# Kernel tuning notes

Measured on AMD Instinct MI355X. Metric: run time of the kernel, lower is better.

## Reference

```python
import jax, jax.numpy as jnp
import numpy as np

EMBED = 512
NHEAD = 16
HDIM = EMBED // NHEAD
HIDDEN = 512  # Mlp hidden is hard-coded to 512
EPS_LN = 1e-6
EPS_ATT = 1e-6


def layernorm(x, gamma, beta):
    mu = jnp.mean(x, axis=-1, keepdims=True)
    var = jnp.mean(jnp.square(x - mu), axis=-1, keepdims=True)
    return (x - mu) * jax.lax.rsqrt(var + EPS_LN) * gamma + beta


def setup_inputs() -> dict:
    key = jax.random.key(0)
    ks = jax.random.split(key, 16)
    B, N, C = 8, 4096, EMBED
    s = 1.0 / np.sqrt(C)
    inp = {
        "x": jax.random.normal(ks[0], (B, N, C), dtype=jnp.float32),
        # projection weights stored as (in, out); torch Linear uses x @ W.T
        "Wq": jax.random.normal(ks[1], (C, C), dtype=jnp.float32) * s,
        "Wk": jax.random.normal(ks[2], (C, C), dtype=jnp.float32) * s,
        "Wv": jax.random.normal(ks[3], (C, C), dtype=jnp.float32) * s,
        "Wm": jax.random.normal(ks[4], (C, C), dtype=jnp.float32) * s,
        "W1": jax.random.normal(ks[5], (C, HIDDEN), dtype=jnp.float32) * s,
        "b1": jax.random.normal(ks[6], (HIDDEN,), dtype=jnp.float32) * 1e-6,
        "W2": jax.random.normal(ks[7], (HIDDEN, C), dtype=jnp.float32) * (1.0 / np.sqrt(HIDDEN)),
        "b2": jax.random.normal(ks[8], (C,), dtype=jnp.float32) * 1e-6,
        "g_att": jnp.ones((C,), dtype=jnp.float32),
        "b_att": jnp.zeros((C,), dtype=jnp.float32),
        "g_ffn": jnp.ones((C,), dtype=jnp.float32),
        "b_ffn": jnp.zeros((C,), dtype=jnp.float32),
    }
    return inp


def reference(x, Wq, Wk, Wv, Wm, W1, b1, W2, b2, g_att, b_att, g_ffn, b_ffn):
    B, N, C = x.shape
    # --- attention sub-block ---
    h = layernorm(x, g_att, b_att)
    q = (h @ Wq).reshape(B, N, NHEAD, HDIM)
    k = (h @ Wk).reshape(B, N, NHEAD, HDIM)
    v = (h @ Wv).reshape(B, N, NHEAD, HDIM)
    Q = jax.nn.elu(q) + 1.0  # feature map: elu(x)+1
    K = jax.nn.elu(k) + 1.0
    v = v / N
    KV = jnp.einsum('nshd,nshv->nhdv', K, v)
    Z = 1.0 / (jnp.einsum('nlhd,nhd->nlh', Q, K.sum(axis=1)) + EPS_ATT)
    msg = jnp.einsum('nlhd,nhdv->nlhv', Q, KV) * Z[..., None] * N
    msg = msg.reshape(B, N, C) @ Wm
    x = x + msg
    # --- feed-forward sub-block ---
    h2 = layernorm(x, g_ffn, b_ffn)
    f = jax.nn.gelu(h2 @ W1 + b1, approximate=False) @ W2 + b2
    return x + f
```

## Files before the change

### kernel.cpp

```cpp
#include <hip/hip_runtime.h>
#include <hip/hip_bf16.h>
#include <math.h>

typedef unsigned short u16;
typedef __attribute__((ext_vector_type(8))) __bf16 bf16x8;
typedef __attribute__((ext_vector_type(4))) float floatx4;

#define SEQ   4096
#define BATCH 8
#define ROWS  32768
#define C     512
#define NH    16
#define HD    32

__device__ inline u16 f2bf(float f) {
    union { float f; unsigned u; } v; v.f = f;
    unsigned r = (v.u + 0x7FFFu + ((v.u >> 16) & 1u)) >> 16;
    return (u16)r;
}
__device__ inline float bf2f(u16 h) {
    union { unsigned u; float f; } v; v.u = ((unsigned)h) << 16;
    return v.f;
}

__device__ inline void g2lds16(const u16* g, u16* l) {
    __builtin_amdgcn_global_load_lds((const __attribute__((address_space(1))) unsigned*)g,
                                     (__attribute__((address_space(3))) unsigned*)l, 16, 0, 0);
}

__global__ __launch_bounds__(256) void prep_weights(
    const float* __restrict__ Wq, const float* __restrict__ Wk,
    const float* __restrict__ Wv, const float* __restrict__ Wm,
    const float* __restrict__ W1, const float* __restrict__ W2,
    u16* __restrict__ Wqkvt, u16* __restrict__ Wmt,
    u16* __restrict__ W1t, u16* __restrict__ W2t)
{
    int blk = blockIdx.x;
    int mat = blk >> 6;
    int tile = blk & 63;
    int k0 = (tile >> 3) * 64, n0 = (tile & 7) * 64;
    const float* src; u16* dst;
    switch (mat) {
        case 0: src = Wq; dst = Wqkvt;              break;
        case 1: src = Wk; dst = Wqkvt + 512*512;    break;
        case 2: src = Wv; dst = Wqkvt + 2*512*512;  break;
        case 3: src = Wm; dst = Wmt;                break;
        case 4: src = W1; dst = W1t;                break;
        default: src = W2; dst = W2t;               break;
    }
    __shared__ float ts[64][65];
    int t = threadIdx.x;
    #pragma unroll
    for (int i = 0; i < 16; i++) {
        int e = i * 256 + t;
        int kr = e >> 6, nc = e & 63;
        ts[kr][nc] = src[(size_t)(k0 + kr) * 512 + n0 + nc];
    }
    __syncthreads();
    #pragma unroll
    for (int i = 0; i < 2; i++) {
        int e = i * 256 + t;
        int nr = e >> 3, kc0 = (e & 7) * 8;
        union { uint4 v; u16 u[8]; } o;
        #pragma unroll
        for (int q = 0; q < 8; q++) o.u[q] = f2bf(ts[kc0 + q][nr]);
        *(uint4*)(dst + (size_t)(n0 + nr) * 512 + k0 + kc0) = o.v;
    }
}

__global__ __launch_bounds__(256) void ln_kernel(
    const float* __restrict__ in, const float* __restrict__ g,
    const float* __restrict__ b, u16* __restrict__ out)
{
    int row  = blockIdx.x * 4 + (threadIdx.x >> 6);
    int lane = threadIdx.x & 63;
    const float* p = in + (size_t)row * C + lane * 8;
    float4 v0 = *(const float4*)p;
    float4 v1 = *(const float4*)(p + 4);
    float s  = v0.x + v0.y + v0.z + v0.w + v1.x + v1.y + v1.z + v1.w;
    float s2 = v0.x*v0.x + v0.y*v0.y + v0.z*v0.z + v0.w*v0.w
             + v1.x*v1.x + v1.y*v1.y + v1.z*v1.z + v1.w*v1.w;
    #pragma unroll
    for (int off = 1; off < 64; off <<= 1) {
        s  += __shfl_xor(s, off);
        s2 += __shfl_xor(s2, off);
    }
    float mean = s * (1.f / C);
    float var  = s2 * (1.f / C) - mean * mean;
    float inv  = rsqrtf(var + 1e-6f);
    int c = lane * 8;
    float4 g0 = *(const float4*)(g + c), g1 = *(const float4*)(g + c + 4);
    float4 b0 = *(const float4*)(b + c), b1 = *(const float4*)(b + c + 4);
    union { uint4 v; u16 u[8]; } o;
    o.u[0] = f2bf((v0.x - mean) * inv * g0.x + b0.x);
    o.u[1] = f2bf((v0.y - mean) * inv * g0.y + b0.y);
    o.u[2] = f2bf((v0.z - mean) * inv * g0.z + b0.z);
    o.u[3] = f2bf((v0.w - mean) * inv * g0.w + b0.w);
    o.u[4] = f2bf((v1.x - mean) * inv * g1.x + b1.x);
    o.u[5] = f2bf((v1.y - mean) * inv * g1.y + b1.y);
    o.u[6] = f2bf((v1.z - mean) * inv * g1.z + b1.z);
    o.u[7] = f2bf((v1.w - mean) * inv * g1.w + b1.w);
    *(uint4*)(out + (size_t)row * C + c) = o.v;
}

template <int EPI>
__global__ __launch_bounds__(256, 2) void gemm_tile(
    const u16* __restrict__ A, const u16* __restrict__ Bt,
    int K, int ldc,
    u16* __restrict__ outb, float* __restrict__ outf,
    const float* __restrict__ bias, const float* __restrict__ resid)
{
    __shared__ u16 lsA[128 * 64];
    __shared__ u16 lsB[128 * 64];
    const int t = threadIdx.x;
    const int w = t >> 6, l = t & 63, lr = l & 15, quad = l >> 4;
    const int m0 = blockIdx.y * 128, n0 = blockIdx.x * 128;
    const int RW = (w >> 1) * 64, CW = (w & 1) * 64;

    floatx4 acc[4][4];
    #pragma unroll
    for (int i = 0; i < 4; i++)
        #pragma unroll
        for (int j = 0; j < 4; j++) { floatx4 z = {0.f, 0.f, 0.f, 0.f}; acc[i][j] = z; }

    const int srow = w * 32 + (l >> 3);
    const int scol = (((l & 7) - (l >> 3)) & 7) * 8;
    const u16* Ag = A  + (size_t)(m0 + srow) * K + scol;
    const u16* Bg = Bt + (size_t)(n0 + srow) * K + scol;
    u16* lAw = lsA + w * 2048;
    u16* lBw = lsB + w * 2048;

    for (int kk = 0; kk < K; kk += 64) {
        __syncthreads();
        #pragma unroll
        for (int c = 0; c < 4; c++) {
            g2lds16(Ag + (size_t)(c * 8) * K + kk, lAw + c * 512);
            g2lds16(Bg + (size_t)(c * 8) * K + kk, lBw + c * 512);
        }
        __syncthreads();
        #pragma unroll
        for (int ks = 0; ks < 2; ks++) {
            bf16x8 af[4], bfr[4];
            const int m = ((ks * 4 + quad + (lr & 7)) & 7) * 8;
            #pragma unroll
            for (int i = 0; i < 4; i++) {
                af[i]  = *(const bf16x8*)(lsA + (RW + i * 16 + lr) * 64 + m);
                bfr[i] = *(const bf16x8*)(lsB + (CW + i * 16 + lr) * 64 + m);
            }
            #pragma unroll
            for (int i = 0; i < 4; i++)
                #pragma unroll
                for (int j = 0; j < 4; j++)
                    acc[i][j] = __builtin_amdgcn_mfma_f32_16x16x32_bf16(af[i], bfr[j], acc[i][j], 0, 0, 0);
        }
    }

    #pragma unroll
    for (int i = 0; i < 4; i++) {
        #pragma unroll
        for (int j = 0; j < 4; j++) {
            #pragma unroll
            for (int r = 0; r < 4; r++) {
                int row = m0 + RW + i * 16 + quad * 4 + r;
                int col = n0 + CW + j * 16 + lr;
                float v = acc[i][j][r];
                size_t idx = (size_t)row * ldc + col;
                if constexpr (EPI == 0) {
                    if (col < 1024) v = v > 0.f ? v + 1.f : __expf(v);
                    else            v *= (1.0f / SEQ);
                    outb[idx] = f2bf(v);
                } else if constexpr (EPI == 1) {
                    outf[idx] = resid[idx] + v;
                } else if constexpr (EPI == 2) {
                    v += bias[col];
                    v = 0.5f * v * (1.f + erff(v * 0.70710678118f));
                    outb[idx] = f2bf(v);
                } else {
                    outf[idx] = outf[idx] + v + bias[col];
                }
            }
        }
    }
}

__global__ __launch_bounds__(256) void kv_reduce(
    const u16* __restrict__ qkv, float* __restrict__ KV, float* __restrict__ Ksum)
{
    int bh = blockIdx.x;
    int b = bh >> 4, h = bh & 15;
    int chunk = blockIdx.y;
    int t = threadIdx.x;
    __shared__ float Ks[32 * 32];
    __shared__ float Vs[32 * 32];
    int d  = t & 31;
    int vd = (t >> 5) << 2;
    float a0 = 0.f, a1 = 0.f, a2 = 0.f, a3 = 0.f, ks = 0.f;
    const size_t base = (size_t)b * SEQ * 1536 + 512 + h * HD;
    int j   = t & 127;
    int isV = t >> 7;
    int sl  = j >> 2, cc = (j & 3) * 8;
    float* dst = (isV ? Vs : Ks) + sl * 32 + cc;
    for (int so = 0; so < 256; so += 32) {
        size_t gp = base + (size_t)(chunk * 256 + so + sl) * 1536 + cc + (isV ? 512 : 0);
        union { uint4 v; u16 u[8]; } uu;
        uu.v = *(const uint4*)(qkv + gp);
        float f[8];
        #pragma unroll
        for (int q = 0; q < 8; q++) f[q] = bf2f(uu.u[q]);
        __syncthreads();
        *(float4*)dst       = float4{f[0], f[1], f[2], f[3]};
        *(float4*)(dst + 4) = float4{f[4], f[5], f[6], f[7]};
        __syncthreads();
        #pragma unroll
        for (int s = 0; s < 32; s++) {
            float kvv = Ks[s * 32 + d];
            float4 vv = *(const float4*)(Vs + s * 32 + vd);
            a0 += kvv * vv.x; a1 += kvv * vv.y; a2 += kvv * vv.z; a3 += kvv * vv.w;
            ks += kvv;
        }
    }
    float* kvp = KV + (size_t)bh * 1024 + d * 32 + vd;
    atomicAdd(kvp + 0, a0);
    atomicAdd(kvp + 1, a1);
    atomicAdd(kvp + 2, a2);
    atomicAdd(kvp + 3, a3);
    if (t < 32) atomicAdd(Ksum + bh * 32 + t, ks);
}

__global__ __launch_bounds__(256) void msg_kernel(
    const u16* __restrict__ qkv, const float* __restrict__ KV,
    const float* __restrict__ Ksum, u16* __restrict__ msg)
{
    int blk = blockIdx.x;
    int b = blk >> 7;
    int r0 = (blk & 127) * 32;
    int t = threadIdx.x;
    int h = t >> 4;
    int vd = (t & 15) * 2;
    float kv0[32], kv1[32], ksr[32];
    const float* kvh = KV + ((size_t)b * 16 + h) * 1024;
    const float* ksh = Ksum + (b * 16 + h) * 32;
    #pragma unroll
    for (int d = 0; d < 32; d++) {
        kv0[d] = kvh[d * 32 + vd];
        kv1[d] = kvh[d * 32 + vd + 1];
        ksr[d] = ksh[d];
    }
    __shared__ u16 Qs[4 * 512];
    const int srr = t >> 6;
    const int scc = (t & 63) * 8;
    for (int rg = 0; rg < 32; rg += 4) {
        size_t row = (size_t)b * SEQ + r0 + rg;
        uint4 qv = *(const uint4*)(qkv + (row + srr) * 1536 + scc);
        __syncthreads();
        *(uint4*)(Qs + srr * 512 + scc) = qv;
        __syncthreads();
        #pragma unroll
        for (int r2 = 0; r2 < 4; r2++) {
            const u16* qp = Qs + r2 * 512 + h * HD;
            float q[32];
            #pragma unroll
            for (int i0 = 0; i0 < 32; i0 += 8) {
                union { uint4 v; u16 u[8]; } uu;
                uu.v = *(const uint4*)(qp + i0);
                #pragma unroll
                for (int jq = 0; jq < 8; jq++) q[i0 + jq] = bf2f(uu.u[jq]);
            }
            float zdot = 0.f, m0 = 0.f, m1 = 0.f;
            #pragma unroll
            for (int d = 0; d < 32; d++) {
                float qd = q[d];
                zdot += qd * ksr[d];
                m0   += qd * kv0[d];
                m1   += qd * kv1[d];
            }
            float z = (float)SEQ / (zdot + 1e-6f);
            unsigned pack = (unsigned)f2bf(m0 * z) | ((unsigned)f2bf(m1 * z) << 16);
            *(unsigned*)(msg + (row + r2) * C + h * HD + vd) = pack;
        }
    }
}

extern "C" void kernel_launch(void* const* d_in, const int* in_sizes, int n_in,
                              void* d_out, int out_size, void* d_ws, size_t ws_size,
                              hipStream_t stream) {
    const float* x     = (const float*)d_in[0];
    const float* Wq    = (const float*)d_in[1];
    const float* Wk    = (const float*)d_in[2];
    const float* Wv    = (const float*)d_in[3];
    const float* Wm    = (const float*)d_in[4];
    const float* W1    = (const float*)d_in[5];
    const float* b1    = (const float*)d_in[6];
    const float* W2    = (const float*)d_in[7];
    const float* b2    = (const float*)d_in[8];
    const float* g_att = (const float*)d_in[9];
    const float* b_att = (const float*)d_in[10];
    const float* g_ffn = (const float*)d_in[11];
    const float* b_ffn = (const float*)d_in[12];
    float* out = (float*)d_out;

    char* ws = (char*)d_ws;
    u16*   Wqkvt = (u16*)(ws);
    u16*   Wmt   = (u16*)(ws + 0x180000);
    u16*   W1t   = (u16*)(ws + 0x200000);
    u16*   W2t   = (u16*)(ws + 0x280000);
    float* KV    = (float*)(ws + 0x300000);
    float* Ksum  = (float*)(ws + 0x380000);
    u16*   hb    = (u16*)(ws + 0x400000);
    u16*   qkv   = (u16*)(ws + 0x2400000);
    u16*   h2    = qkv;
    u16*   f1    = (u16*)(ws + 0x4400000);

    prep_weights<<<6 * 64, 256, 0, stream>>>(Wq, Wk, Wv, Wm, W1, W2,
                                             Wqkvt, Wmt, W1t, W2t);
    ln_kernel<<<ROWS / 4, 256, 0, stream>>>(x, g_att, b_att, hb);
    gemm_tile<0><<<dim3(12, 256), 256, 0, stream>>>(hb, Wqkvt, 512, 1536,
                                                    qkv, nullptr, nullptr, nullptr);
    hipMemsetAsync(KV, 0, (128 * 1024 + 128 * 32) * sizeof(float), stream);
    kv_reduce<<<dim3(128, 16), 256, 0, stream>>>(qkv, KV, Ksum);
    msg_kernel<<<1024, 256, 0, stream>>>(qkv, KV, Ksum, hb);
    gemm_tile<1><<<dim3(4, 256), 256, 0, stream>>>(hb, Wmt, 512, 512,
                                                   nullptr, out, nullptr, x);
    ln_kernel<<<ROWS / 4, 256, 0, stream>>>(out, g_ffn, b_ffn, h2);
    gemm_tile<2><<<dim3(4, 256), 256, 0, stream>>>(h2, W1t, 512, 512,
                                                   f1, nullptr, b1, nullptr);
    gemm_tile<3><<<dim3(4, 256), 256, 0, stream>>>(f1, W2t, 512, 512,
                                                   nullptr, out, b2, nullptr);
}
```

Baseline: 445.3 us.

## Compute K^T V reduction with bf16 MFMA and deterministic two-stage partial sums

Rewrites kv_reduce to load K and V tiles straight into LDS through a double-buffered async path (g2lds16) and to compute the per-chunk K^T V product with 16x16x32 bf16 MFMA instructions, replacing the scalar FMA loop over fp32 shared tiles. Each wave writes its partial KV and Ksum to a workspace buffer instead of using atomicAdd, and a new kv_final kernel sums the 32 partials per head. This removes the memset and the atomic contention. The cost is an extra kernel launch and partial-sum traffic, and the partial buffer overlaps the hb region (hb is dead at that point).

```diff
diff --git a/kernel.cpp b/kernel.cpp
--- a/kernel.cpp
+++ b/kernel.cpp
@@ -184,47 +184,110 @@
 }
 
 __global__ __launch_bounds__(256) void kv_reduce(
-    const u16* __restrict__ qkv, float* __restrict__ KV, float* __restrict__ Ksum)
-{
-    int bh = blockIdx.x;
-    int b = bh >> 4, h = bh & 15;
-    int chunk = blockIdx.y;
-    int t = threadIdx.x;
-    __shared__ float Ks[32 * 32];
-    __shared__ float Vs[32 * 32];
-    int d  = t & 31;
-    int vd = (t >> 5) << 2;
-    float a0 = 0.f, a1 = 0.f, a2 = 0.f, a3 = 0.f, ks = 0.f;
-    const size_t base = (size_t)b * SEQ * 1536 + 512 + h * HD;
-    int j   = t & 127;
-    int isV = t >> 7;
-    int sl  = j >> 2, cc = (j & 3) * 8;
-    float* dst = (isV ? Vs : Ks) + sl * 32 + cc;
-    for (int so = 0; so < 256; so += 32) {
-        size_t gp = base + (size_t)(chunk * 256 + so + sl) * 1536 + cc + (isV ? 512 : 0);
-        union { uint4 v; u16 u[8]; } uu;
-        uu.v = *(const uint4*)(qkv + gp);
-        float f[8];
-        #pragma unroll
-        for (int q = 0; q < 8; q++) f[q] = bf2f(uu.u[q]);
-        __syncthreads();
-        *(float4*)dst       = float4{f[0], f[1], f[2], f[3]};
-        *(float4*)(dst + 4) = float4{f[4], f[5], f[6], f[7]};
-        __syncthreads();
-        #pragma unroll
-        for (int s = 0; s < 32; s++) {
-            float kvv = Ks[s * 32 + d];
-            float4 vv = *(const float4*)(Vs + s * 32 + vd);
-            a0 += kvv * vv.x; a1 += kvv * vv.y; a2 += kvv * vv.z; a3 += kvv * vv.w;
-            ks += kvv;
-        }
-    }
-    float* kvp = KV + (size_t)bh * 1024 + d * 32 + vd;
-    atomicAdd(kvp + 0, a0);
-    atomicAdd(kvp + 1, a1);
-    atomicAdd(kvp + 2, a2);
-    atomicAdd(kvp + 3, a3);
-    if (t < 32) atomicAdd(Ksum + bh * 32 + t, ks);
+    const u16* __restrict__ qkv, float* __restrict__ Pkv, float* __restrict__ PKsum)
+{
+    const int bh = blockIdx.x;
+    const int b = bh >> 4, h = bh & 15;
+    const int chunk = blockIdx.y;
+    const int t = threadIdx.x;
+    const int w = t >> 6, l = t & 63, lr = l & 15, quad = l >> 4;
+    __shared__ u16 lds[4 * 2 * 2048];
+
+    const int sbase = chunk * 512 + w * 128;
+    const u16* qbase = qkv + (size_t)b * SEQ * 1536 + 512 + h * HD;
+
+    const int sl0 = l >> 2;
+    const int sl1 = 16 + sl0;
+    const int cl  = l & 3;
+    const int cg0 = (cl + (sl0 >> 3)) & 3;
+    const int cg1 = (cl + (sl1 >> 3)) & 3;
+    const int gof0 = sl0 * 1536 + cg0 * 8;
+    const int gof1 = sl1 * 1536 + cg1 * 8;
+
+    u16* myl = lds + w * 4096;
+
+    const int offA0 = quad * 256 + ((((lr >> 3) + 0) - quad) & 3) * 8 + (lr & 7);
+    const int offA1 = quad * 256 + ((((lr >> 3) + 2) - quad) & 3) * 8 + (lr & 7);
+
+    floatx4 a00 = {0,0,0,0}, a01 = {0,0,0,0}, a10 = {0,0,0,0}, a11 = {0,0,0,0};
+    float ks0 = 0.f, ks1 = 0.f;
+
+    {
+        const u16* gK = qbase + (size_t)sbase * 1536;
+        g2lds16(gK + gof0,       myl);
+        g2lds16(gK + gof1,       myl + 512);
+        g2lds16(gK + 512 + gof0, myl + 1024);
+        g2lds16(gK + 512 + gof1, myl + 1536);
+    }
+    #pragma unroll
+    for (int st = 0; st < 4; st++) {
+        if (st < 3) {
+            const u16* gK = qbase + (size_t)(sbase + (st + 1) * 32) * 1536;
+            u16* nl = myl + ((st + 1) & 1) * 2048;
+            g2lds16(gK + gof0,       nl);
+            g2lds16(gK + gof1,       nl + 512);
+            g2lds16(gK + 512 + gof0, nl + 1024);
+            g2lds16(gK + 512 + gof1, nl + 1536);
+        }
+        __syncthreads();
+        const u16* lK = myl + (st & 1) * 2048;
+        const u16* lV = lK + 1024;
+        union { bf16x8 v; u16 u[8]; } fa0, fa1, fb0, fb1;
+        #pragma unroll
+        for (int j = 0; j < 8; j++) {
+            fa0.u[j] = lK[offA0 + j * 32];
+            fa1.u[j] = lK[offA1 + j * 32];
+            fb0.u[j] = lV[offA0 + j * 32];
+            fb1.u[j] = lV[offA1 + j * 32];
+        }
+        #pragma unroll
+        for (int j = 0; j < 8; j++) { ks0 += bf2f(fa0.u[j]); ks1 += bf2f(fa1.u[j]); }
+        a00 = __builtin_amdgcn_mfma_f32_16x16x32_bf16(fa0.v, fb0.v, a00, 0, 0, 0);
+        a01 = __builtin_amdgcn_mfma_f32_16x16x32_bf16(fa0.v, fb1.v, a01, 0, 0, 0);
+        a10 = __builtin_amdgcn_mfma_f32_16x16x32_bf16(fa1.v, fb0.v, a10, 0, 0, 0);
+        a11 = __builtin_amdgcn_mfma_f32_16x16x32_bf16(fa1.v, fb1.v, a11, 0, 0, 0);
+    }
+
+    const int p = bh * 32 + chunk * 4 + w;
+    float* dst = Pkv + (size_t)p * 1024;
+    floatx4 accs[2][2] = {{a00, a01}, {a10, a11}};
+    #pragma unroll
+    for (int i = 0; i < 2; i++)
+        #pragma unroll
+        for (int j = 0; j < 2; j++)
+            #pragma unroll
+            for (int r = 0; r < 4; r++)
+                dst[(i * 16 + quad * 4 + r) * 32 + j * 16 + lr] = accs[i][j][r];
+
+    float k0 = ks0 + __shfl_xor(ks0, 16); k0 += __shfl_xor(k0, 32);
+    float k1 = ks1 + __shfl_xor(ks1, 16); k1 += __shfl_xor(k1, 32);
+    if (quad == 0) {
+        PKsum[p * 32 + lr]      = k0;
+        PKsum[p * 32 + 16 + lr] = k1;
+    }
+}
+
+__global__ __launch_bounds__(256) void kv_final(
+    const float* __restrict__ Pkv, const float* __restrict__ PKsum,
+    float* __restrict__ KV, float* __restrict__ Ksum)
+{
+    const int bh = blockIdx.x;
+    const int t = threadIdx.x;
+    float a0 = 0.f, a1 = 0.f, a2 = 0.f, a3 = 0.f;
+    for (int p = 0; p < 32; p++) {
+        const float* src = Pkv + ((size_t)bh * 32 + p) * 1024;
+        a0 += src[t];
+        a1 += src[t + 256];
+        a2 += src[t + 512];
+        a3 += src[t + 768];
+    }
+    float* dst = KV + (size_t)bh * 1024;
+    dst[t] = a0; dst[t + 256] = a1; dst[t + 512] = a2; dst[t + 768] = a3;
+    if (t < 32) {
+        float s = 0.f;
+        for (int p = 0; p < 32; p++) s += PKsum[(bh * 32 + p) * 32 + t];
+        Ksum[bh * 32 + t] = s;
+    }
 }
 
 __global__ __launch_bounds__(256) void msg_kernel(
@@ -307,6 +370,8 @@
     float* KV    = (float*)(ws + 0x300000);
     float* Ksum  = (float*)(ws + 0x380000);
     u16*   hb    = (u16*)(ws + 0x400000);
+    float* Pkv   = (float*)(ws + 0x400000);
+    float* PKsum = (float*)(ws + 0x1400000);
     u16*   qkv   = (u16*)(ws + 0x2400000);
     u16*   h2    = qkv;
     u16*   f1    = (u16*)(ws + 0x4400000);
@@ -316,8 +381,8 @@
     ln_kernel<<<ROWS / 4, 256, 0, stream>>>(x, g_att, b_att, hb);
     gemm_tile<0><<<dim3(12, 256), 256, 0, stream>>>(hb, Wqkvt, 512, 1536,
                                                     qkv, nullptr, nullptr, nullptr);
-    hipMemsetAsync(KV, 0, (128 * 1024 + 128 * 32) * sizeof(float), stream);
-    kv_reduce<<<dim3(128, 16), 256, 0, stream>>>(qkv, KV, Ksum);
+    kv_reduce<<<dim3(128, 8), 256, 0, stream>>>(qkv, Pkv, PKsum);
+    kv_final<<<128, 256, 0, stream>>>(Pkv, PKsum, KV, Ksum);
     msg_kernel<<<1024, 256, 0, stream>>>(qkv, KV, Ksum, hb);
     gemm_tile<1><<<dim3(4, 256), 256, 0, stream>>>(hb, Wmt, 512, 512,
                                                    nullptr, out, nullptr, x);
```

New measurement: 412.4 us. 1.08x faster.
